# Kernel optimization log

Measured on AMD Instinct MI355X. Metric: run time of the kernel, lower is better.

Reference implementation:

```python
import jax, jax.numpy as jnp
import numpy as np

N_NODES = 100000
N_EDGES = 1600000
IN_DIM = 256
HEADS = 4
OUT_DIM = 32
NEG_SLOPE = 0.2


def setup_inputs() -> dict:
    key = jax.random.key(0)
    ks = jax.random.split(key, 6)
    x = jax.random.normal(ks[0], (N_NODES, IN_DIM), dtype=jnp.float32)
    # xavier-ish init scale for fc and attention vectors
    W = jax.random.normal(ks[1], (IN_DIM, HEADS * OUT_DIM), dtype=jnp.float32) * (1.0 / np.sqrt(IN_DIM))
    attn_l = jax.random.normal(ks[2], (HEADS, OUT_DIM), dtype=jnp.float32) * (1.0 / np.sqrt(OUT_DIM))
    attn_r = jax.random.normal(ks[3], (HEADS, OUT_DIM), dtype=jnp.float32) * (1.0 / np.sqrt(OUT_DIM))
    src = jax.random.randint(ks[4], (N_EDGES,), 0, N_NODES, dtype=jnp.int32)
    dst = jax.random.randint(ks[5], (N_EDGES,), 0, N_NODES, dtype=jnp.int32)
    return {"x": x, "W": W, "attn_l": attn_l, "attn_r": attn_r, "src": src, "dst": dst}


def reference(x, W, attn_l, attn_r, src, dst):
    N = x.shape[0]
    H, D = attn_l.shape
    # shared linear projection (feat_drop = 0)
    feat = (x @ W).reshape(N, H, D)                      # [N,H,D]
    el = jnp.sum(feat * attn_l, axis=-1)                 # [N,H]
    er = jnp.sum(feat * attn_r, axis=-1)                 # [N,H]
    e = jax.nn.leaky_relu(el[src] + er[dst], NEG_SLOPE)  # [E,H]
    # edge softmax over incoming edges of each destination node
    m = jax.ops.segment_max(e, dst, num_segments=N)      # [N,H]
    m = jnp.where(jnp.isfinite(m), m, 0.0)               # zero-in-degree guard
    ex = jnp.exp(e - m[dst])                             # [E,H]
    denom = jax.ops.segment_sum(ex, dst, num_segments=N) # [N,H]
    a = ex / jnp.maximum(denom[dst], 1e-9)               # [E,H] (attn_drop = 0)
    # weighted scatter-add aggregation
    out = jax.ops.segment_sum(a[:, :, None] * feat[src], dst, num_segments=N)  # [N,H,D]
    # head mean (the .mean(1) in GAT1.forward)
    return out.mean(axis=1)                              # [N,D]
```

## Files before the change

kernel.cpp:

```cpp
#include <hip/hip_runtime.h>
#include <math.h>

#define NN 100000
#define NE 1600000
#define IN_DIM 256
#define HD 128
#define NEG_SLOPE 0.2f

#define B1SH 9
#define NPB (1 << B1SH)
#define NB1 ((NN + NPB - 1) / NPB)
#define SC_BLOCKS ((NE / 4 + 1023) / 1024)
#define DBK 64

typedef __attribute__((ext_vector_type(8))) __bf16 bf16x8;
typedef __attribute__((ext_vector_type(4))) float floatx4;

__device__ inline unsigned short f2bf(float f) {
    unsigned int b = __float_as_uint(f);
    b += 0x7fffu + ((b >> 16) & 1u);
    return (unsigned short)(b >> 16);
}
__device__ inline unsigned int pk(float lo, float hi) {
    return (unsigned int)f2bf(lo) | ((unsigned int)f2bf(hi) << 16);
}
__device__ inline float bflo(unsigned int u) { return __uint_as_float(u << 16); }
__device__ inline float bfhi(unsigned int u) { return __uint_as_float(u & 0xffff0000u); }
__device__ inline float lrelu(float v) { return (v > 0.f) ? v : v * NEG_SLOPE; }

__global__ __launch_bounds__(256) void prep_w_kernel(const float* __restrict__ W,
                                                     unsigned int* __restrict__ wswz) {
    int g = blockIdx.x * 256 + threadIdx.x;
    int lane = g & 63;
    int t = (g >> 6) & 7;
    int c = g >> 9;
    int sub = lane & 15, quad = lane >> 4;
    int n = t * 16 + sub;
    int kbase = c * 32 + quad * 8;
    unsigned int ob = (unsigned int)g * 4;
#pragma unroll
    for (int i = 0; i < 4; ++i) {
        float lo = W[(size_t)(kbase + 2 * i) * HD + n];
        float hi = W[(size_t)(kbase + 2 * i + 1) * HD + n];
        wswz[ob + i] = pk(lo, hi);
    }
}

__global__ __launch_bounds__(256, 4) void gemm_kernel(const float* __restrict__ x,
                                                      const uint4* __restrict__ wswz,
                                                      const float* __restrict__ attn_l,
                                                      const float* __restrict__ attn_r,
                                                      unsigned short* __restrict__ featb,
                                                      float* __restrict__ el,
                                                      float* __restrict__ er) {
    const int tid = threadIdx.x;
    const int lane = tid & 63, wv = tid >> 6;
    const int sub = lane & 15, quad = lane >> 4;
    const int row0 = blockIdx.x * 64 + wv * 16;

    int m = row0 + sub;
    if (m >= NN) m = NN - 1;
    const float* xp = x + (size_t)m * IN_DIM + quad * 8;

    bf16x8 af[8];
#pragma unroll
    for (int h = 0; h < 2; ++h) {
        float4 raw[4][2];
#pragma unroll
        for (int c = 0; c < 4; ++c) {
            raw[c][0] = *(const float4*)(xp + (h * 4 + c) * 32);
            raw[c][1] = *(const float4*)(xp + (h * 4 + c) * 32 + 4);
        }
#pragma unroll
        for (int c = 0; c < 4; ++c) {
            uint4 au;
            au.x = pk(raw[c][0].x, raw[c][0].y);
            au.y = pk(raw[c][0].z, raw[c][0].w);
            au.z = pk(raw[c][1].x, raw[c][1].y);
            au.w = pk(raw[c][1].z, raw[c][1].w);
            af[h * 4 + c] = __builtin_bit_cast(bf16x8, au);
        }
    }

    floatx4 acc[8];
#pragma unroll
    for (int t = 0; t < 8; ++t) acc[t] = (floatx4){0.f, 0.f, 0.f, 0.f};

#pragma unroll
    for (int c = 0; c < 8; ++c) {
        uint4 bu[8];
#pragma unroll
        for (int t = 0; t < 8; ++t) bu[t] = wswz[(c * 8 + t) * 64 + lane];
#pragma unroll
        for (int t = 0; t < 8; ++t) {
            bf16x8 bfr = __builtin_bit_cast(bf16x8, bu[t]);
            acc[t] = __builtin_amdgcn_mfma_f32_16x16x32_bf16(af[c], bfr, acc[t], 0, 0, 0);
        }
    }

    float al[8], ar[8];
#pragma unroll
    for (int t = 0; t < 8; ++t) {
        al[t] = attn_l[t * 16 + sub];
        ar[t] = attn_r[t * 16 + sub];
    }

#pragma unroll
    for (int r = 0; r < 4; ++r) {
        int row = row0 + quad * 4 + r;
        uint4 fv;
        fv.x = pk(acc[0][r], acc[1][r]);
        fv.y = pk(acc[2][r], acc[3][r]);
        fv.z = pk(acc[4][r], acc[5][r]);
        fv.w = pk(acc[6][r], acc[7][r]);
        float pl[4], pr[4];
#pragma unroll
        for (int hh = 0; hh < 4; ++hh) {
            pl[hh] = acc[2 * hh][r] * al[2 * hh] + acc[2 * hh + 1][r] * al[2 * hh + 1];
            pr[hh] = acc[2 * hh][r] * ar[2 * hh] + acc[2 * hh + 1][r] * ar[2 * hh + 1];
        }
#pragma unroll
        for (int o = 1; o < 16; o <<= 1) {
#pragma unroll
            for (int hh = 0; hh < 4; ++hh) {
                pl[hh] += __shfl_xor(pl[hh], o);
                pr[hh] += __shfl_xor(pr[hh], o);
            }
        }
        if (row < NN) {
            *(uint4*)(featb + (size_t)row * HD + sub * 8) = fv;
            if (sub < 4) {
                float vl = (sub == 0) ? pl[0] : (sub == 1) ? pl[1] : (sub == 2) ? pl[2] : pl[3];
                float vr = (sub == 0) ? pr[0] : (sub == 1) ? pr[1] : (sub == 2) ? pr[2] : pr[3];
                el[row * 4 + sub] = vl;
                er[row * 4 + sub] = vr;
            }
        }
    }
}

__global__ __launch_bounds__(256) void precount_kernel(const int4* __restrict__ dst4,
                                                       int* __restrict__ gbcnt) {
    __shared__ int cnt[NB1];
    int t = threadIdx.x;
    for (int i = t; i < NB1; i += 256) cnt[i] = 0;
    __syncthreads();
    int base4 = blockIdx.x * 1024;
#pragma unroll
    for (int k = 0; k < 4; ++k) {
        int gi = base4 + k * 256 + t;
        if (gi < NE / 4) {
            int4 d = dst4[gi];
            atomicAdd(&cnt[d.x >> B1SH], 1);
            atomicAdd(&cnt[d.y >> B1SH], 1);
            atomicAdd(&cnt[d.z >> B1SH], 1);
            atomicAdd(&cnt[d.w >> B1SH], 1);
        }
    }
    __syncthreads();
    for (int i = t; i < NB1; i += 256)
        if (cnt[i]) atomicAdd(&gbcnt[i], cnt[i]);
}

__global__ __launch_bounds__(256) void bscan_kernel(const int* __restrict__ gbcnt,
                                                    int* __restrict__ regstart,
                                                    int* __restrict__ gcursor,
                                                    int* __restrict__ offs) {
    __shared__ int sh[256];
    int t = threadIdx.x;
    int v = (t < NB1) ? gbcnt[t] : 0;
    sh[t] = v;
    __syncthreads();
    for (int o = 1; o < 256; o <<= 1) {
        int a = (t >= o) ? sh[t - o] : 0;
        __syncthreads();
        sh[t] += a;
        __syncthreads();
    }
    int excl = sh[t] - v;
    if (t < NB1) {
        regstart[t] = excl;
        gcursor[t] = excl;
    }
    if (t == 0) {
        regstart[NB1] = NE;
        offs[NN] = NE;
    }
}

__global__ __launch_bounds__(256) void scatter_kernel(const int4* __restrict__ src4,
                                                      const int4* __restrict__ dst4,
                                                      int* __restrict__ gcursor,
                                                      unsigned int* __restrict__ pkd) {
    __shared__ int cnt[NB1];
    __shared__ int gbase[NB1];
    int t = threadIdx.x;
    for (int i = t; i < NB1; i += 256) cnt[i] = 0;
    __syncthreads();

    int base4 = blockIdx.x * 1024;
    unsigned int pkv[16];
    unsigned int brk[16];
#pragma unroll
    for (int k = 0; k < 4; ++k) {
        int gi = base4 + k * 256 + t;
        bool ok = gi < NE / 4;
        int gic = ok ? gi : 0;
        int4 s = src4[gic];
        int4 d = dst4[gic];
        int dd[4] = {d.x, d.y, d.z, d.w};
        int ss[4] = {s.x, s.y, s.z, s.w};
#pragma unroll
        for (int j4 = 0; j4 < 4; ++j4) {
            int e = k * 4 + j4;
            if (ok) {
                int b = dd[j4] >> B1SH;
                int r = atomicAdd(&cnt[b], 1);
                brk[e] = ((unsigned int)b << 12) | (unsigned int)r;
                pkv[e] = ((unsigned int)(dd[j4] & (NPB - 1)) << 17) | (unsigned int)ss[j4];
            } else {
                brk[e] = 0xFFFFFFFFu;
            }
        }
    }
    __syncthreads();
    for (int i = t; i < NB1; i += 256)
        gbase[i] = cnt[i] ? atomicAdd(&gcursor[i], cnt[i]) : 0;
    __syncthreads();
#pragma unroll
    for (int e = 0; e < 16; ++e) {
        if (brk[e] != 0xFFFFFFFFu) {
            int b = brk[e] >> 12;
            int r = brk[e] & 0xFFF;
            pkd[gbase[b] + r] = pkv[e];
        }
    }
}

__global__ __launch_bounds__(256) void build_kernel(const unsigned int* __restrict__ pkd,
                                                    const int* __restrict__ regstart,
                                                    int* __restrict__ offs,
                                                    int* __restrict__ csr_src,
                                                    int* __restrict__ dcnt) {
    __shared__ int fcnt[NPB];
    __shared__ int foffs[NPB];
    __shared__ int ssc[256];
    __shared__ int dh[DBK];
    int b = blockIdx.x, t = threadIdx.x;
    int rs = regstart[b], re = regstart[b + 1];
    int n = re - rs;

    for (int i = t; i < NPB; i += 256) fcnt[i] = 0;
    if (t < DBK) dh[t] = 0;
    __syncthreads();
    for (int i = t; i < n; i += 256) {
        unsigned int v = pkd[rs + i];
        atomicAdd(&fcnt[v >> 17], 1);
    }
    __syncthreads();
    int a0 = fcnt[2 * t], a1 = fcnt[2 * t + 1];
    {
        int node0 = b * NPB + 2 * t;
        if (node0 < NN)     atomicAdd(&dh[a0 < DBK ? a0 : DBK - 1], 1);
        if (node0 + 1 < NN) atomicAdd(&dh[a1 < DBK ? a1 : DBK - 1], 1);
    }
    int s = a0 + a1;
    ssc[t] = s;
    __syncthreads();
    for (int o = 1; o < 256; o <<= 1) {
        int u = (t >= o) ? ssc[t - o] : 0;
        __syncthreads();
        ssc[t] += u;
        __syncthreads();
    }
    int excl = ssc[t] - s;
    foffs[2 * t] = excl;
    foffs[2 * t + 1] = excl + a0;
    __syncthreads();
    if (t < DBK && dh[t]) atomicAdd(&dcnt[t], dh[t]);
#pragma unroll
    for (int q = 0; q < 2; ++q) {
        int j = t + q * 256;
        int node = b * NPB + j;
        if (node < NN) offs[node] = rs + foffs[j];
    }
    for (int i = t; i < NPB; i += 256) fcnt[i] = 0;
    __syncthreads();
    int i = t;
    for (; i + 768 < n; i += 1024) {
        unsigned int v0 = pkd[rs + i];
        unsigned int v1 = pkd[rs + i + 256];
        unsigned int v2 = pkd[rs + i + 512];
        unsigned int v3 = pkd[rs + i + 768];
        int j0 = v0 >> 17, j1 = v1 >> 17, j2 = v2 >> 17, j3 = v3 >> 17;
        int r0 = atomicAdd(&fcnt[j0], 1);
        int r1 = atomicAdd(&fcnt[j1], 1);
        int r2 = atomicAdd(&fcnt[j2], 1);
        int r3 = atomicAdd(&fcnt[j3], 1);
        csr_src[rs + foffs[j0] + r0] = (int)(v0 & 0x1FFFFu);
        csr_src[rs + foffs[j1] + r1] = (int)(v1 & 0x1FFFFu);
        csr_src[rs + foffs[j2] + r2] = (int)(v2 & 0x1FFFFu);
        csr_src[rs + foffs[j3] + r3] = (int)(v3 & 0x1FFFFu);
    }
    for (; i < n; i += 256) {
        unsigned int v = pkd[rs + i];
        int j = v >> 17;
        int r = atomicAdd(&fcnt[j], 1);
        csr_src[rs + foffs[j] + r] = (int)(v & 0x1FFFFu);
    }
}

__global__ void degscan_kernel(const int* __restrict__ dcnt, int* __restrict__ dcur) {
    int t = threadIdx.x;
    int v = dcnt[t];
    int s = v;
#pragma unroll
    for (int o = 1; o < 64; o <<= 1) {
        int u = __shfl_up(s, o);
        if (t >= o) s += u;
    }
    dcur[t] = s - v;
}

__global__ __launch_bounds__(256) void permfill_kernel(const int* __restrict__ offs,
                                                       int* __restrict__ dcur,
                                                       int* __restrict__ perm) {
    __shared__ int c[DBK], base[DBK];
    int t = threadIdx.x;
    if (t < DBK) c[t] = 0;
    __syncthreads();
    int n = blockIdx.x * 256 + t;
    int d = 0, r = 0;
    bool ok = n < NN;
    if (ok) {
        d = offs[n + 1] - offs[n];
        if (d > DBK - 1) d = DBK - 1;
        r = atomicAdd(&c[d], 1);
    }
    __syncthreads();
    if (t < DBK) base[t] = c[t] ? atomicAdd(&dcur[t], c[t]) : 0;
    __syncthreads();
    if (ok) perm[base[d] + r] = n;
}

#define CH 32
__global__ __launch_bounds__(256, 4) void aggregate_kernel(const uint4* __restrict__ featu4,
                                                           const float4* __restrict__ el4,
                                                           const float4* __restrict__ er4,
                                                           const int* __restrict__ offs,
                                                           const int* __restrict__ csr_src,
                                                           const int* __restrict__ perm,
                                                           float* __restrict__ out) {
    __shared__ int    s_sv[4][4][CH];
    __shared__ float4 s_a4[4][4][CH];

    const int tid = threadIdx.x;
    const int lane = tid & 63, wv = tid >> 6;
    const int g = lane >> 4, sub = lane & 15;
    const int node = perm[blockIdx.x * 16 + wv * 4 + g];
    const int beg = offs[node], end = offs[node + 1];

    const float4 erv = er4[node];
    float4 sm = make_float4(0.f, 0.f, 0.f, 0.f);
    float acc[8];
#pragma unroll
    for (int i = 0; i < 8; ++i) acc[i] = 0.f;

    for (int c0 = beg; c0 < end; c0 += CH) {
        int cnt = end - c0;
        if (cnt > CH) cnt = CH;
#pragma unroll
        for (int t = 0; t < 2; ++t) {
            int slot = sub + t * 16;
            int sv = 0;
            float4 w = make_float4(0.f, 0.f, 0.f, 0.f);
            if (slot < cnt) {
                sv = csr_src[c0 + slot];
                float4 e = el4[sv];
                w.x = __expf(lrelu(e.x + erv.x));
                w.y = __expf(lrelu(e.y + erv.y));
                w.z = __expf(lrelu(e.z + erv.z));
                w.w = __expf(lrelu(e.w + erv.w));
                sm.x += w.x; sm.y += w.y; sm.z += w.z; sm.w += w.w;
            }
            s_sv[wv][g][slot] = sv;
            s_a4[wv][g][slot] = w;
        }
        int rounds = (cnt + 7) >> 3;
        for (int jr = 0; jr < rounds; ++jr) {
            int jb = jr << 3;
            int sv[8];
#pragma unroll
            for (int e = 0; e < 8; ++e) sv[e] = s_sv[wv][g][jb + e];
            uint4 u[8];
#pragma unroll
            for (int e = 0; e < 8; ++e) u[e] = featu4[(size_t)sv[e] * 16 + sub];
            float4 w[8];
#pragma unroll
            for (int e = 0; e < 8; ++e) w[e] = s_a4[wv][g][jb + e];
#pragma unroll
            for (int e = 0; e < 8; ++e) {
                acc[0] = fmaf(w[e].x, bflo(u[e].x), acc[0]);
                acc[1] = fmaf(w[e].x, bfhi(u[e].x), acc[1]);
                acc[2] = fmaf(w[e].y, bflo(u[e].y), acc[2]);
                acc[3] = fmaf(w[e].y, bfhi(u[e].y), acc[3]);
                acc[4] = fmaf(w[e].z, bflo(u[e].z), acc[4]);
                acc[5] = fmaf(w[e].z, bfhi(u[e].z), acc[5]);
                acc[6] = fmaf(w[e].w, bflo(u[e].w), acc[6]);
                acc[7] = fmaf(w[e].w, bfhi(u[e].w), acc[7]);
            }
        }
    }

#pragma unroll
    for (int o = 1; o < 16; o <<= 1) {
        sm.x += __shfl_xor(sm.x, o);
        sm.y += __shfl_xor(sm.y, o);
        sm.z += __shfl_xor(sm.z, o);
        sm.w += __shfl_xor(sm.w, o);
    }
    float ix = 1.f / fmaxf(sm.x, 1e-9f);
    float iy = 1.f / fmaxf(sm.y, 1e-9f);
    float iz = 1.f / fmaxf(sm.z, 1e-9f);
    float iw = 1.f / fmaxf(sm.w, 1e-9f);
    float ox = 0.25f * (acc[0] * ix + acc[2] * iy + acc[4] * iz + acc[6] * iw);
    float oy = 0.25f * (acc[1] * ix + acc[3] * iy + acc[5] * iz + acc[7] * iw);
    out[node * 32 + sub]      = ox;
    out[node * 32 + 16 + sub] = oy;
}

extern "C" void kernel_launch(void* const* d_in, const int* in_sizes, int n_in,
                              void* d_out, int out_size, void* d_ws, size_t ws_size,
                              hipStream_t stream) {
    const float* x      = (const float*)d_in[0];
    const float* W      = (const float*)d_in[1];
    const float* attn_l = (const float*)d_in[2];
    const float* attn_r = (const float*)d_in[3];
    const int*   src    = (const int*)d_in[4];
    const int*   dst    = (const int*)d_in[5];
    float* out = (float*)d_out;

    char* p = (char*)d_ws;
    auto alloc = [&](size_t bytes) -> void* {
        void* r = (void*)p;
        p += (bytes + 255) & ~(size_t)255;
        return r;
    };
    unsigned short* featb = (unsigned short*)alloc((size_t)NN * HD * 2);
    unsigned int*   wswz  = (unsigned int*)alloc(4096 * 16);
    float* el      = (float*)alloc((size_t)NN * 4 * 4);
    float* er      = (float*)alloc((size_t)NN * 4 * 4);
    int*   offs    = (int*)alloc((size_t)(NN + 1) * 4);
    unsigned int* pkd = (unsigned int*)alloc((size_t)NE * 4);
    int*   csr     = (int*)alloc((size_t)NE * 4);
    int*   gbcnt   = (int*)alloc((size_t)NB1 * 4);
    int*   regstart= (int*)alloc((size_t)(NB1 + 1) * 4);
    int*   gcursor = (int*)alloc((size_t)NB1 * 4);
    int*   dcnt    = (int*)alloc((size_t)DBK * 4);
    int*   dcur    = (int*)alloc((size_t)DBK * 4);
    int*   perm    = (int*)alloc((size_t)NN * 4);

    hipMemsetAsync(gbcnt, 0, (size_t)NB1 * 4, stream);
    hipMemsetAsync(dcnt, 0, (size_t)DBK * 4, stream);

    prep_w_kernel<<<16, 256, 0, stream>>>(W, wswz);
    gemm_kernel<<<(NN + 63) / 64, 256, 0, stream>>>(x, (const uint4*)wswz, attn_l, attn_r,
                                                    featb, el, er);
    precount_kernel<<<SC_BLOCKS, 256, 0, stream>>>((const int4*)dst, gbcnt);
    bscan_kernel<<<1, 256, 0, stream>>>(gbcnt, regstart, gcursor, offs);
    scatter_kernel<<<SC_BLOCKS, 256, 0, stream>>>((const int4*)src, (const int4*)dst,
                                                  gcursor, pkd);
    build_kernel<<<NB1, 256, 0, stream>>>(pkd, regstart, offs, csr, dcnt);
    degscan_kernel<<<1, 64, 0, stream>>>(dcnt, dcur);
    permfill_kernel<<<(NN + 255) / 256, 256, 0, stream>>>(offs, dcur, perm);
    aggregate_kernel<<<NN / 16, 256, 0, stream>>>((const uint4*)featb, (const float4*)el,
                                                  (const float4*)er, offs, csr, perm, out);
}
```

Before: 319.6 us.

## Replace global degree-sort permutation with per-block local degree ranking in aggregate

Removes the global degree histogram, the degscan kernel and the permfill kernel that built a degree-sorted node permutation. The aggregate kernel now ranks its own 16 nodes by degree in shared memory and maps them to wavefront groups, which balances work within a block but not across the grid. It also pads the shared arrays to CH+1 and drops the occupancy hint in launch_bounds on the gemm and aggregate kernels. This saves two launches and some global atomics, at the risk of more load imbalance across blocks.

```diff
diff --git a/kernel.cpp b/kernel.cpp
--- a/kernel.cpp
+++ b/kernel.cpp
@@ -11,7 +11,6 @@
 #define NPB (1 << B1SH)
 #define NB1 ((NN + NPB - 1) / NPB)
 #define SC_BLOCKS ((NE / 4 + 1023) / 1024)
-#define DBK 64
 
 typedef __attribute__((ext_vector_type(8))) __bf16 bf16x8;
 typedef __attribute__((ext_vector_type(4))) float floatx4;
@@ -46,13 +45,13 @@
     }
 }
 
-__global__ __launch_bounds__(256, 4) void gemm_kernel(const float* __restrict__ x,
-                                                      const uint4* __restrict__ wswz,
-                                                      const float* __restrict__ attn_l,
-                                                      const float* __restrict__ attn_r,
-                                                      unsigned short* __restrict__ featb,
-                                                      float* __restrict__ el,
-                                                      float* __restrict__ er) {
+__global__ __launch_bounds__(256) void gemm_kernel(const float* __restrict__ x,
+                                                   const uint4* __restrict__ wswz,
+                                                   const float* __restrict__ attn_l,
+                                                   const float* __restrict__ attn_r,
+                                                   unsigned short* __restrict__ featb,
+                                                   float* __restrict__ el,
+                                                   float* __restrict__ er) {
     const int tid = threadIdx.x;
     const int lane = tid & 63, wv = tid >> 6;
     const int sub = lane & 15, quad = lane >> 4;
@@ -240,18 +239,15 @@
 __global__ __launch_bounds__(256) void build_kernel(const unsigned int* __restrict__ pkd,
                                                     const int* __restrict__ regstart,
                                                     int* __restrict__ offs,
-                                                    int* __restrict__ csr_src,
-                                                    int* __restrict__ dcnt) {
+                                                    int* __restrict__ csr_src) {
     __shared__ int fcnt[NPB];
     __shared__ int foffs[NPB];
     __shared__ int ssc[256];
-    __shared__ int dh[DBK];
     int b = blockIdx.x, t = threadIdx.x;
     int rs = regstart[b], re = regstart[b + 1];
     int n = re - rs;
 
     for (int i = t; i < NPB; i += 256) fcnt[i] = 0;
-    if (t < DBK) dh[t] = 0;
     __syncthreads();
     for (int i = t; i < n; i += 256) {
         unsigned int v = pkd[rs + i];
@@ -259,11 +255,6 @@
     }
     __syncthreads();
     int a0 = fcnt[2 * t], a1 = fcnt[2 * t + 1];
-    {
-        int node0 = b * NPB + 2 * t;
-        if (node0 < NN)     atomicAdd(&dh[a0 < DBK ? a0 : DBK - 1], 1);
-        if (node0 + 1 < NN) atomicAdd(&dh[a1 < DBK ? a1 : DBK - 1], 1);
-    }
     int s = a0 + a1;
     ssc[t] = s;
     __syncthreads();
@@ -277,7 +268,6 @@
     foffs[2 * t] = excl;
     foffs[2 * t + 1] = excl + a0;
     __syncthreads();
-    if (t < DBK && dh[t]) atomicAdd(&dcnt[t], dh[t]);
 #pragma unroll
     for (int q = 0; q < 2; ++q) {
         int j = t + q * 256;
@@ -310,54 +300,38 @@
     }
 }
 
-__global__ void degscan_kernel(const int* __restrict__ dcnt, int* __restrict__ dcur) {
-    int t = threadIdx.x;
-    int v = dcnt[t];
-    int s = v;
-#pragma unroll
-    for (int o = 1; o < 64; o <<= 1) {
-        int u = __shfl_up(s, o);
-        if (t >= o) s += u;
-    }
-    dcur[t] = s - v;
-}
-
-__global__ __launch_bounds__(256) void permfill_kernel(const int* __restrict__ offs,
-                                                       int* __restrict__ dcur,
-                                                       int* __restrict__ perm) {
-    __shared__ int c[DBK], base[DBK];
-    int t = threadIdx.x;
-    if (t < DBK) c[t] = 0;
-    __syncthreads();
-    int n = blockIdx.x * 256 + t;
-    int d = 0, r = 0;
-    bool ok = n < NN;
-    if (ok) {
-        d = offs[n + 1] - offs[n];
-        if (d > DBK - 1) d = DBK - 1;
-        r = atomicAdd(&c[d], 1);
-    }
-    __syncthreads();
-    if (t < DBK) base[t] = c[t] ? atomicAdd(&dcur[t], c[t]) : 0;
-    __syncthreads();
-    if (ok) perm[base[d] + r] = n;
-}
-
 #define CH 32
-__global__ __launch_bounds__(256, 4) void aggregate_kernel(const uint4* __restrict__ featu4,
-                                                           const float4* __restrict__ el4,
-                                                           const float4* __restrict__ er4,
-                                                           const int* __restrict__ offs,
-                                                           const int* __restrict__ csr_src,
-                                                           const int* __restrict__ perm,
-                                                           float* __restrict__ out) {
-    __shared__ int    s_sv[4][4][CH];
-    __shared__ float4 s_a4[4][4][CH];
+__global__ __launch_bounds__(256) void aggregate_kernel(const uint4* __restrict__ featu4,
+                                                        const float4* __restrict__ el4,
+                                                        const float4* __restrict__ er4,
+                                                        const int* __restrict__ offs,
+                                                        const int* __restrict__ csr_src,
+                                                        float* __restrict__ out) {
+    __shared__ int    s_sv[4][4][CH + 1];
+    __shared__ float4 s_a4[4][4][CH + 1];
+    __shared__ int sdeg[16], smap[16];
 
     const int tid = threadIdx.x;
     const int lane = tid & 63, wv = tid >> 6;
     const int g = lane >> 4, sub = lane & 15;
-    const int node = perm[blockIdx.x * 16 + wv * 4 + g];
+
+    if (tid < 16) {
+        int n0 = blockIdx.x * 16 + tid;
+        sdeg[tid] = offs[n0 + 1] - offs[n0];
+    }
+    __syncthreads();
+    if (tid < 16) {
+        int d = sdeg[tid];
+        int rank = 0;
+#pragma unroll
+        for (int j = 0; j < 16; ++j) {
+            int dj = sdeg[j];
+            rank += (dj < d) || (dj == d && j < tid);
+        }
+        smap[rank] = blockIdx.x * 16 + tid;
+    }
+    __syncthreads();
+    const int node = smap[wv * 4 + g];
     const int beg = offs[node], end = offs[node + 1];
 
     const float4 erv = er4[node];
@@ -456,12 +430,8 @@
     int*   gbcnt   = (int*)alloc((size_t)NB1 * 4);
     int*   regstart= (int*)alloc((size_t)(NB1 + 1) * 4);
     int*   gcursor = (int*)alloc((size_t)NB1 * 4);
-    int*   dcnt    = (int*)alloc((size_t)DBK * 4);
-    int*   dcur    = (int*)alloc((size_t)DBK * 4);
-    int*   perm    = (int*)alloc((size_t)NN * 4);
 
     hipMemsetAsync(gbcnt, 0, (size_t)NB1 * 4, stream);
-    hipMemsetAsync(dcnt, 0, (size_t)DBK * 4, stream);
 
     prep_w_kernel<<<16, 256, 0, stream>>>(W, wswz);
     gemm_kernel<<<(NN + 63) / 64, 256, 0, stream>>>(x, (const uint4*)wswz, attn_l, attn_r,
@@ -470,9 +440,7 @@
     bscan_kernel<<<1, 256, 0, stream>>>(gbcnt, regstart, gcursor, offs);
     scatter_kernel<<<SC_BLOCKS, 256, 0, stream>>>((const int4*)src, (const int4*)dst,
                                                   gcursor, pkd);
-    build_kernel<<<NB1, 256, 0, stream>>>(pkd, regstart, offs, csr, dcnt);
-    degscan_kernel<<<1, 64, 0, stream>>>(dcnt, dcur);
-    permfill_kernel<<<(NN + 255) / 256, 256, 0, stream>>>(offs, dcur, perm);
+    build_kernel<<<NB1, 256, 0, stream>>>(pkd, regstart, offs, csr);
     aggregate_kernel<<<NN / 16, 256, 0, stream>>>((const uint4*)featb, (const float4*)el,
-                                                  (const float4*)er, offs, csr, perm, out);
-}
+                                                  (const float4*)er, offs, csr, out);
+}
```

Measured after the change: 302.1 us. -5.5%, faster.
